# Kernel tuning notes

Hardware: AMD Instinct MI355X
Metric: run time of the kernel (lower is better)

## Reference

```python
import jax, jax.numpy as jnp
import numpy as np

D_MODEL = 1024
NUM_HEADS = 16
D_K = D_MODEL // NUM_HEADS


def setup_inputs() -> dict:
    key = jax.random.key(0)
    ks = jax.random.split(key, 12)
    B, S, D = 2, 2048, D_MODEL
    s = 1.0 / np.sqrt(D)
    inp = {
        "Q": jax.random.normal(ks[0], (B, S, D), jnp.float32),
        "K": jax.random.normal(ks[1], (B, S, D), jnp.float32),
        "V": jax.random.normal(ks[2], (B, S, D), jnp.float32),
        "Wq": jax.random.normal(ks[3], (D, D), jnp.float32) * s,
        "bq": jax.random.normal(ks[4], (D,), jnp.float32) * s,
        "Wk": jax.random.normal(ks[5], (D, D), jnp.float32) * s,
        "bk": jax.random.normal(ks[6], (D,), jnp.float32) * s,
        "Wv": jax.random.normal(ks[7], (D, D), jnp.float32) * s,
        "bv": jax.random.normal(ks[8], (D,), jnp.float32) * s,
        "Wo": jax.random.normal(ks[9], (D, D), jnp.float32) * s,
        "bo": jax.random.normal(ks[10], (D,), jnp.float32) * s,
    }
    return inp


def _split_heads(x, B, S):
    # [B, S, D] -> [B, H, S, d_k]
    return x.reshape(B, S, NUM_HEADS, D_K).transpose(0, 2, 1, 3)


def reference(Q, K, V, Wq, bq, Wk, bk, Wv, bv, Wo, bo):
    B, S, D = Q.shape
    # torch nn.Linear: y = x @ W.T + b
    q = _split_heads(Q @ Wq.T + bq, B, S)
    k = _split_heads(K @ Wk.T + bk, B, S)
    v = _split_heads(V @ Wv.T + bv, B, S)
    scale = 1.0 / np.sqrt(D_K).astype(np.float32)
    # [B, H, S, S] attention scores (materialized, as in the original)
    scores = jnp.einsum('bhqd,bhkd->bhqk', q, k) * scale
    probs = jax.nn.softmax(scores, axis=-1)
    out = jnp.einsum('bhqk,bhkd->bhqd', probs, v)
    out = out.transpose(0, 2, 1, 3).reshape(B, S, D)
    return out @ Wo.T + bo
```

## Files before the change

### kernel.cpp

```cpp
#include <hip/hip_runtime.h>
#include <hip/hip_bf16.h>

#define S_LEN   2048
#define NHEADS  16
#define DKH     64
#define DMODEL  1024
#define NBATCH  2

typedef __bf16 bf16x8 __attribute__((ext_vector_type(8)));
typedef __bf16 bf16x4 __attribute__((ext_vector_type(4)));
typedef float  f32x4  __attribute__((ext_vector_type(4)));

typedef __attribute__((address_space(3))) void       lds_void;
typedef const __attribute__((address_space(1))) void glob_void;

__device__ __forceinline__ void glds16(const void* g, void* l) {
    __builtin_amdgcn_global_load_lds((glob_void*)g, (lds_void*)l, 16, 0, 0);
}

struct CvtArgs {
    const float* src[7];
    __bf16*      dst[7];
    int          n[7];
};

__global__ __launch_bounds__(256)
void cvt_all_k(CvtArgs a)
{
    const int t = blockIdx.y;
    const size_t i = ((size_t)blockIdx.x * 256 + threadIdx.x) * 8;
    if ((int)i >= a.n[t]) return;
    const float* s = a.src[t];
    f32x4 lo = *(const f32x4*)(s + i);
    f32x4 hi = *(const f32x4*)(s + i + 4);
    bf16x8 r;
#pragma unroll
    for (int k = 0; k < 4; ++k) { r[k] = (__bf16)lo[k]; r[4 + k] = (__bf16)hi[k]; }
    *(bf16x8*)(a.dst[t] + i) = r;
}

__device__ __forceinline__ void gemm_core(
    const __bf16* __restrict__ A, const __bf16* __restrict__ W,
    int m0, int n0, int K,
    __bf16 (*As)[32], __bf16 (*Ws)[32], f32x4 acc[4][4])
{
    const int tid  = threadIdx.x;
    const int lane = tid & 63;
    const int wv   = tid >> 6;
    const int l15  = lane & 15;
    const int quad = lane >> 4;
    const int wm   = wv >> 1;
    const int wn   = wv & 1;
    const int grow = lane >> 2;
    const int gcol = (lane & 3) * 8;

    const __bf16* ag0 = A + (size_t)(m0 + wv * 32 + grow) * K + gcol;
    const __bf16* ag1 = A + (size_t)(m0 + wv * 32 + 16 + grow) * K + gcol;
    const __bf16* wg0 = W + (size_t)(n0 + wv * 32 + grow) * K + gcol;
    const __bf16* wg1 = W + (size_t)(n0 + wv * 32 + 16 + grow) * K + gcol;
    void* al0 = &As[wv * 32][0];
    void* al1 = &As[wv * 32 + 16][0];
    void* wl0 = &Ws[wv * 32][0];
    void* wl1 = &Ws[wv * 32 + 16][0];

    for (int k0 = 0;;) {
        __syncthreads();
        glds16(ag0 + k0, al0);
        glds16(ag1 + k0, al1);
        glds16(wg0 + k0, wl0);
        glds16(wg1 + k0, wl1);
        __syncthreads();

        bf16x8 af[4], wf[4];
#pragma unroll
        for (int i = 0; i < 4; ++i)
            af[i] = *(const bf16x8*)&As[wm * 64 + i * 16 + l15][quad * 8];
#pragma unroll
        for (int j = 0; j < 4; ++j)
            wf[j] = *(const bf16x8*)&Ws[wn * 64 + j * 16 + l15][quad * 8];
#pragma unroll
        for (int i = 0; i < 4; ++i)
#pragma unroll
            for (int j = 0; j < 4; ++j)
                acc[i][j] = __builtin_amdgcn_mfma_f32_16x16x32_bf16(af[i], wf[j], acc[i][j], 0, 0, 0);

        k0 += 32;
        if (k0 >= K) break;
    }
}

struct GArgs {
    const __bf16* A[3];
    const __bf16* W[3];
    const float*  bias[3];
    __bf16*       out[3];
};

__global__ __launch_bounds__(256)
void gemm_qkv(GArgs g, int z_off)
{
    __shared__ __align__(16) __bf16 As[128][32];
    __shared__ __align__(16) __bf16 Ws[128][32];

    const int fid = blockIdx.x;
    const int z   = (fid >> 8) + z_off;
    const int l   = fid & 255;
    const int x   = l & 7;
    const int t   = l >> 3;
    int m0, n0;
    if (z == 2) { m0 = (t & 7) * 128;          n0 = (x * 4 + (t >> 3)) * 128; }
    else        { m0 = (x * 4 + (t & 3)) * 128; n0 = (t >> 2) * 128; }

    f32x4 acc[4][4];
#pragma unroll
    for (int i = 0; i < 4; ++i)
#pragma unroll
        for (int j = 0; j < 4; ++j) acc[i][j] = (f32x4){0.f, 0.f, 0.f, 0.f};

    gemm_core(g.A[z], g.W[z], m0, n0, DMODEL, As, Ws, acc);

    const int lane = threadIdx.x & 63;
    const int wv   = threadIdx.x >> 6;
    const int l15  = lane & 15;
    const int quad = lane >> 4;
    const int wm   = wv >> 1;
    const int wn   = wv & 1;
    const float* bias = g.bias[z];
    __bf16* out = g.out[z];
    const float oscale = (z == 0) ? 0.125f : 1.0f;

#pragma unroll
    for (int j = 0; j < 4; ++j) {
        const int col = n0 + wn * 64 + j * 16 + l15;
        const float bcol = (z == 2) ? 0.f : bias[col];
#pragma unroll
        for (int i = 0; i < 4; ++i) {
#pragma unroll
            for (int r = 0; r < 4; ++r) {
                const int row = m0 + wm * 64 + i * 16 + quad * 4 + r;
                size_t idx;
                float v = acc[i][j][r];
                if (z == 2) {
                    const int h = row >> 6, d = row & (DKH - 1);
                    const int b = col >> 11, s = col & (S_LEN - 1);
                    v += bias[row];
                    idx = ((size_t)(b * NHEADS + h) * DKH + d) * S_LEN + s;
                } else {
                    const int b = row >> 11, s = row & (S_LEN - 1);
                    const int h = col >> 6, d = col & (DKH - 1);
                    v = (v + bcol) * oscale;
                    idx = ((size_t)(b * NHEADS + h) * S_LEN + s) * DKH + d;
                }
                out[idx] = (__bf16)v;
            }
        }
    }
}

__global__ __launch_bounds__(256)
void gemm_out(const __bf16* __restrict__ A, const __bf16* __restrict__ W,
              const float* __restrict__ bias, float* __restrict__ out)
{
    __shared__ __align__(16) __bf16 As[128][32];
    __shared__ __align__(16) __bf16 Ws[128][32];

    const int fid = blockIdx.x;
    const int x = fid & 7;
    const int t = fid >> 3;
    const int m0 = (x * 4 + (t & 3)) * 128;
    const int n0 = (t >> 2) * 128;

    f32x4 acc[4][4];
#pragma unroll
    for (int i = 0; i < 4; ++i)
#pragma unroll
        for (int j = 0; j < 4; ++j) acc[i][j] = (f32x4){0.f, 0.f, 0.f, 0.f};

    gemm_core(A, W, m0, n0, DMODEL, As, Ws, acc);

    const int lane = threadIdx.x & 63;
    const int wv   = threadIdx.x >> 6;
    const int l15  = lane & 15;
    const int quad = lane >> 4;
    const int wm   = wv >> 1;
    const int wn   = wv & 1;

#pragma unroll
    for (int j = 0; j < 4; ++j) {
        const int col = n0 + wn * 64 + j * 16 + l15;
        const float bv = bias[col];
#pragma unroll
        for (int i = 0; i < 4; ++i)
#pragma unroll
            for (int r = 0; r < 4; ++r) {
                const int row = m0 + wm * 64 + i * 16 + quad * 4 + r;
                out[(size_t)row * DMODEL + col] = acc[i][j][r] + bv;
            }
    }
}

__global__ __launch_bounds__(256, 2)
void attn_k(const __bf16* __restrict__ Qh, const __bf16* __restrict__ Kh,
            const __bf16* __restrict__ VhT, __bf16* __restrict__ out)
{
    __shared__ __align__(16) __bf16 Ks[128][72];
    __shared__ __align__(16) __bf16 Vs[64][136];

    const int tid  = threadIdx.x;
    const int lane = tid & 63;
    const int wv   = tid >> 6;
    const int l15  = lane & 15;
    const int quad = lane >> 4;

    const int fid = blockIdx.x;
    const int x  = fid & 7;
    const int j  = fid >> 3;
    const int bh = x * 4 + (j & 3);
    const int q0 = (j >> 2) * 128;
    const int b  = bh >> 4;
    const int h  = bh & (NHEADS - 1);

    const __bf16* Q  = Qh  + (size_t)bh * S_LEN * DKH;
    const __bf16* Kp = Kh  + (size_t)bh * S_LEN * DKH;
    const __bf16* Vt = VhT + (size_t)bh * DKH * S_LEN;

    bf16x8 qa[2][2];
#pragma unroll
    for (int u = 0; u < 2; ++u) {
        const int qrow = q0 + wv * 32 + u * 16 + l15;
        qa[u][0] = *(const bf16x8*)(Q + (size_t)qrow * DKH + quad * 8);
        qa[u][1] = *(const bf16x8*)(Q + (size_t)qrow * DKH + quad * 8 + 32);
    }

    const int krow = tid >> 1, kcb = (tid & 1) * 32;
    const int vrow = tid >> 2, vcb = (tid & 3) * 32;
    const __bf16* kst = Kp + (size_t)krow * DKH   + kcb;
    const __bf16* vst = Vt + (size_t)vrow * S_LEN + vcb;

    f32x4 oT[2][4];
#pragma unroll
    for (int u = 0; u < 2; ++u)
#pragma unroll
        for (int jt = 0; jt < 4; ++jt) oT[u][jt] = (f32x4){0.f, 0.f, 0.f, 0.f};
    float lacc[2] = {0.f, 0.f};

    bf16x8 kreg[4], vperm[4];
    {
        bf16x8 vr[4];
#pragma unroll
        for (int p = 0; p < 4; ++p) {
            kreg[p] = *(const bf16x8*)(kst + p * 8);
            vr[p]   = *(const bf16x8*)(vst + p * 8);
        }
#pragma unroll
        for (int p = 0; p < 4; ++p) {
            const int G = (p >> 1), e = (p & 1) * 4;
#pragma unroll
            for (int s = 0; s < 4; ++s) {
                vperm[p][s]     = vr[G][e + s];
                vperm[p][4 + s] = vr[G + 2][e + s];
            }
        }
    }

    for (int kt = 0; kt < S_LEN; kt += 128) {
        __syncthreads();
#pragma unroll
        for (int p = 0; p < 4; ++p) {
            *(bf16x8*)&Ks[krow][kcb + p * 8] = kreg[p];
            *(bf16x8*)&Vs[vrow][vcb + p * 8] = vperm[p];
        }
        __syncthreads();
        if (kt + 128 < S_LEN) {
            bf16x8 vr[4];
#pragma unroll
            for (int p = 0; p < 4; ++p) {
                kreg[p] = *(const bf16x8*)(kst + (size_t)(kt + 128) * DKH + p * 8);
                vr[p]   = *(const bf16x8*)(vst + kt + 128 + p * 8);
            }
#pragma unroll
            for (int p = 0; p < 4; ++p) {
                const int G = (p >> 1), e = (p & 1) * 4;
#pragma unroll
                for (int s = 0; s < 4; ++s) {
                    vperm[p][s]     = vr[G][e + s];
                    vperm[p][4 + s] = vr[G + 2][e + s];
                }
            }
        }

#pragma unroll
        for (int ht = 0; ht < 2; ++ht) {
            float p[2][4][4];
#pragma unroll
            for (int n = 0; n < 4; ++n) {
                bf16x8 kA = *(const bf16x8*)&Ks[ht * 64 + n * 16 + l15][quad * 8];
                bf16x8 kB = *(const bf16x8*)&Ks[ht * 64 + n * 16 + l15][quad * 8 + 32];
#pragma unroll
                for (int u = 0; u < 2; ++u) {
                    f32x4 st = {0.f, 0.f, 0.f, 0.f};
                    st = __builtin_amdgcn_mfma_f32_16x16x32_bf16(kA, qa[u][0], st, 0, 0, 0);
                    st = __builtin_amdgcn_mfma_f32_16x16x32_bf16(kB, qa[u][1], st, 0, 0, 0);
#pragma unroll
                    for (int r = 0; r < 4; ++r) {
                        p[u][n][r] = __expf(st[r]);
                        lacc[u] += p[u][n][r];
                    }
                }
            }

#pragma unroll
            for (int t = 0; t < 2; ++t) {
                bf16x8 pf[2];
#pragma unroll
                for (int u = 0; u < 2; ++u)
#pragma unroll
                    for (int s = 0; s < 4; ++s) {
                        pf[u][s]     = (__bf16)p[u][2 * t][s];
                        pf[u][4 + s] = (__bf16)p[u][2 * t + 1][s];
                    }
#pragma unroll
                for (int jt = 0; jt < 4; ++jt) {
                    bf16x8 vf = *(const bf16x8*)&Vs[jt * 16 + l15][ht * 64 + t * 32 + quad * 8];
#pragma unroll
                    for (int u = 0; u < 2; ++u)
                        oT[u][jt] = __builtin_amdgcn_mfma_f32_16x16x32_bf16(vf, pf[u], oT[u][jt], 0, 0, 0);
                }
            }
        }
    }

#pragma unroll
    for (int u = 0; u < 2; ++u) {
        float l = lacc[u];
        l += __shfl_xor(l, 16);
        l += __shfl_xor(l, 32);
        const float inv = 1.0f / l;
        __bf16* op = out + ((size_t)b * S_LEN + q0 + wv * 32 + u * 16 + l15) * DMODEL + h * DKH;
#pragma unroll
        for (int jt = 0; jt < 4; ++jt) {
            bf16x4 t;
#pragma unroll
            for (int r = 0; r < 4; ++r) t[r] = (__bf16)(oT[u][jt][r] * inv);
            *(bf16x4*)(op + jt * 16 + quad * 4) = t;
        }
    }
}

extern "C" void kernel_launch(void* const* d_in, const int* in_sizes, int n_in,
                              void* d_out, int out_size, void* d_ws, size_t ws_size,
                              hipStream_t stream) {
    const float* Qi = (const float*)d_in[0];
    const float* Ki = (const float*)d_in[1];
    const float* Vi = (const float*)d_in[2];
    const float* Wq = (const float*)d_in[3];
    const float* bq = (const float*)d_in[4];
    const float* Wk = (const float*)d_in[5];
    const float* bk = (const float*)d_in[6];
    const float* Wv = (const float*)d_in[7];
    const float* bv = (const float*)d_in[8];
    const float* Wo = (const float*)d_in[9];
    const float* bo = (const float*)d_in[10];
    float* out = (float*)d_out;

    const int M = NBATCH * S_LEN;
    const size_t NW = (size_t)DMODEL * DMODEL;
    const size_t NE = (size_t)M * DMODEL;
    const bool big = ws_size >= ((size_t)56 << 20);

    __bf16* w_bf   = (__bf16*)d_ws;
    __bf16* Qin_bf = w_bf + 4 * NW;
    __bf16* Kin_bf = Qin_bf + NE;
    __bf16* Vin_bf = Kin_bf + NE;
    __bf16* q_ws   = Vin_bf + NE;
    __bf16* k_ws   = q_ws + NE;
    __bf16* vT_ws   = big ? (k_ws + NE) : Kin_bf;
    __bf16* attn_ws = Qin_bf;
    __bf16* wq_bf = w_bf, *wk_bf = w_bf + NW, *wv_bf = w_bf + 2 * NW, *wo_bf = w_bf + 3 * NW;

    CvtArgs ca;
    ca.src[0] = Wq; ca.src[1] = Wk; ca.src[2] = Wv; ca.src[3] = Wo;
    ca.src[4] = Qi; ca.src[5] = Ki; ca.src[6] = Vi;
    ca.dst[0] = wq_bf; ca.dst[1] = wk_bf; ca.dst[2] = wv_bf; ca.dst[3] = wo_bf;
    ca.dst[4] = Qin_bf; ca.dst[5] = Kin_bf; ca.dst[6] = Vin_bf;
    for (int t = 0; t < 4; ++t) ca.n[t] = (int)NW;
    for (int t = 4; t < 7; ++t) ca.n[t] = (int)NE;
    cvt_all_k<<<dim3(2048, 7), 256, 0, stream>>>(ca);

    GArgs g;
    g.A[0] = Qin_bf; g.W[0] = wq_bf;  g.bias[0] = bq; g.out[0] = q_ws;
    g.A[1] = Kin_bf; g.W[1] = wk_bf;  g.bias[1] = bk; g.out[1] = k_ws;
    g.A[2] = wv_bf;  g.W[2] = Vin_bf; g.bias[2] = bv; g.out[2] = vT_ws;
    if (big) {
        gemm_qkv<<<dim3(768), 256, 0, stream>>>(g, 0);
    } else {
        gemm_qkv<<<dim3(512), 256, 0, stream>>>(g, 0);
        gemm_qkv<<<dim3(256), 256, 0, stream>>>(g, 2);
    }

    attn_k<<<dim3(512), 256, 0, stream>>>(q_ws, k_ws, vT_ws, attn_ws);

    gemm_out<<<dim3(256), 256, 0, stream>>>(attn_ws, wo_bf, bo, out);
}
```

Baseline: 246.3 us.

## Fuse fp32-to-bf16 activation conversion into QKV GEMM tile loads

The fp32 activations Q, K and V are no longer converted to bf16 in a separate pass. The QKV GEMM now loads fp32 tiles into registers, prefetching the next k-slice, then converts them and writes bf16 to LDS. The separate conversion kernel shrinks to the weights only, and the workspace layout and the single 768-block launch are simplified. This removes a full read-write pass over about 50 MB of activations. In exchange the GEMM reads fp32 (twice the bytes per tile) and loses the async global-to-LDS path for those operands, and fp32 tiles are re-read by every block along N.

```diff
diff --git a/kernel.cpp b/kernel.cpp
--- a/kernel.cpp
+++ b/kernel.cpp
@@ -18,29 +18,26 @@
     __builtin_amdgcn_global_load_lds((glob_void*)g, (lds_void*)l, 16, 0, 0);
 }
 
-struct CvtArgs {
-    const float* src[7];
-    __bf16*      dst[7];
-    int          n[7];
-};
-
 __global__ __launch_bounds__(256)
-void cvt_all_k(CvtArgs a)
+void cvt_w_k(const float* __restrict__ wq, const float* __restrict__ wk,
+             const float* __restrict__ wv, const float* __restrict__ wo,
+             __bf16* __restrict__ dst)
 {
-    const int t = blockIdx.y;
+    const float* srcs[4] = {wq, wk, wv, wo};
+    const float* s = srcs[blockIdx.y];
+    __bf16* d = dst + (size_t)blockIdx.y * (DMODEL * DMODEL);
     const size_t i = ((size_t)blockIdx.x * 256 + threadIdx.x) * 8;
-    if ((int)i >= a.n[t]) return;
-    const float* s = a.src[t];
     f32x4 lo = *(const f32x4*)(s + i);
     f32x4 hi = *(const f32x4*)(s + i + 4);
     bf16x8 r;
 #pragma unroll
     for (int k = 0; k < 4; ++k) { r[k] = (__bf16)lo[k]; r[4 + k] = (__bf16)hi[k]; }
-    *(bf16x8*)(a.dst[t] + i) = r;
-}
-
+    *(bf16x8*)(d + i) = r;
+}
+
+template<bool AF32, bool WF32>
 __device__ __forceinline__ void gemm_core(
-    const __bf16* __restrict__ A, const __bf16* __restrict__ W,
+    const void* __restrict__ Ap, const void* __restrict__ Wp,
     int m0, int n0, int K,
     __bf16 (*As)[32], __bf16 (*Ws)[32], f32x4 acc[4][4])
 {
@@ -54,22 +51,70 @@
     const int grow = lane >> 2;
     const int gcol = (lane & 3) * 8;
 
-    const __bf16* ag0 = A + (size_t)(m0 + wv * 32 + grow) * K + gcol;
-    const __bf16* ag1 = A + (size_t)(m0 + wv * 32 + 16 + grow) * K + gcol;
-    const __bf16* wg0 = W + (size_t)(n0 + wv * 32 + grow) * K + gcol;
-    const __bf16* wg1 = W + (size_t)(n0 + wv * 32 + 16 + grow) * K + gcol;
+    const __bf16* ag0 = (const __bf16*)Ap + (size_t)(m0 + wv * 32 + grow) * K + gcol;
+    const __bf16* ag1 = (const __bf16*)Ap + (size_t)(m0 + wv * 32 + 16 + grow) * K + gcol;
+    const __bf16* wg0 = (const __bf16*)Wp + (size_t)(n0 + wv * 32 + grow) * K + gcol;
+    const __bf16* wg1 = (const __bf16*)Wp + (size_t)(n0 + wv * 32 + 16 + grow) * K + gcol;
     void* al0 = &As[wv * 32][0];
     void* al1 = &As[wv * 32 + 16][0];
     void* wl0 = &Ws[wv * 32][0];
     void* wl1 = &Ws[wv * 32 + 16][0];
 
+    const int fr = tid >> 1;
+    const int fc = (tid & 1) * 16;
+    const float* afp = (const float*)Ap + (size_t)(m0 + fr) * K + fc;
+    const float* wfp = (const float*)Wp + (size_t)(n0 + fr) * K + fc;
+
+    f32x4 apf[4], wpf[4];
+    if (AF32) {
+#pragma unroll
+        for (int t = 0; t < 4; ++t) apf[t] = *(const f32x4*)(afp + t * 4);
+    }
+    if (WF32) {
+#pragma unroll
+        for (int t = 0; t < 4; ++t) wpf[t] = *(const f32x4*)(wfp + t * 4);
+    }
+
     for (int k0 = 0;;) {
         __syncthreads();
-        glds16(ag0 + k0, al0);
-        glds16(ag1 + k0, al1);
-        glds16(wg0 + k0, wl0);
-        glds16(wg1 + k0, wl1);
+        if (AF32) {
+            bf16x8 v0, v1;
+#pragma unroll
+            for (int t = 0; t < 4; ++t) {
+                v0[t] = (__bf16)apf[0][t]; v0[4 + t] = (__bf16)apf[1][t];
+                v1[t] = (__bf16)apf[2][t]; v1[4 + t] = (__bf16)apf[3][t];
+            }
+            *(bf16x8*)&As[fr][fc]     = v0;
+            *(bf16x8*)&As[fr][fc + 8] = v1;
+        } else {
+            glds16(ag0 + k0, al0);
+            glds16(ag1 + k0, al1);
+        }
+        if (WF32) {
+            bf16x8 v0, v1;
+#pragma unroll
+            for (int t = 0; t < 4; ++t) {
+                v0[t] = (__bf16)wpf[0][t]; v0[4 + t] = (__bf16)wpf[1][t];
+                v1[t] = (__bf16)wpf[2][t]; v1[4 + t] = (__bf16)wpf[3][t];
+            }
+            *(bf16x8*)&Ws[fr][fc]     = v0;
+            *(bf16x8*)&Ws[fr][fc + 8] = v1;
+        } else {
+            glds16(wg0 + k0, wl0);
+            glds16(wg1 + k0, wl1);
+        }
         __syncthreads();
+        k0 += 32;
+        if (k0 < K) {
+            if (AF32) {
+#pragma unroll
+                for (int t = 0; t < 4; ++t) apf[t] = *(const f32x4*)(afp + k0 + t * 4);
+            }
+            if (WF32) {
+#pragma unroll
+                for (int t = 0; t < 4; ++t) wpf[t] = *(const f32x4*)(wfp + k0 + t * 4);
+            }
+        }
 
         bf16x8 af[4], wf[4];
 #pragma unroll
@@ -84,31 +129,30 @@
             for (int j = 0; j < 4; ++j)
                 acc[i][j] = __builtin_amdgcn_mfma_f32_16x16x32_bf16(af[i], wf[j], acc[i][j], 0, 0, 0);
 
-        k0 += 32;
         if (k0 >= K) break;
     }
 }
 
 struct GArgs {
-    const __bf16* A[3];
-    const __bf16* W[3];
-    const float*  bias[3];
-    __bf16*       out[3];
+    const void* A[3];
+    const void* W[3];
+    const float* bias[3];
+    __bf16*     out[3];
 };
 
 __global__ __launch_bounds__(256)
-void gemm_qkv(GArgs g, int z_off)
+void gemm_qkv(GArgs g)
 {
     __shared__ __align__(16) __bf16 As[128][32];
     __shared__ __align__(16) __bf16 Ws[128][32];
 
     const int fid = blockIdx.x;
-    const int z   = (fid >> 8) + z_off;
+    const int z   = fid >> 8;
     const int l   = fid & 255;
     const int x   = l & 7;
     const int t   = l >> 3;
     int m0, n0;
-    if (z == 2) { m0 = (t & 7) * 128;          n0 = (x * 4 + (t >> 3)) * 128; }
+    if (z == 2) { m0 = (t & 7) * 128;           n0 = (x * 4 + (t >> 3)) * 128; }
     else        { m0 = (x * 4 + (t & 3)) * 128; n0 = (t >> 2) * 128; }
 
     f32x4 acc[4][4];
@@ -117,7 +161,8 @@
 #pragma unroll
         for (int j = 0; j < 4; ++j) acc[i][j] = (f32x4){0.f, 0.f, 0.f, 0.f};
 
-    gemm_core(g.A[z], g.W[z], m0, n0, DMODEL, As, Ws, acc);
+    if (z == 2) gemm_core<false, true>(g.A[2], g.W[2], m0, n0, DMODEL, As, Ws, acc);
+    else        gemm_core<true, false>(g.A[z], g.W[z], m0, n0, DMODEL, As, Ws, acc);
 
     const int lane = threadIdx.x & 63;
     const int wv   = threadIdx.x >> 6;
@@ -176,7 +221,7 @@
 #pragma unroll
         for (int j = 0; j < 4; ++j) acc[i][j] = (f32x4){0.f, 0.f, 0.f, 0.f};
 
-    gemm_core(A, W, m0, n0, DMODEL, As, Ws, acc);
+    gemm_core<false, false>(A, W, m0, n0, DMODEL, As, Ws, acc);
 
     const int lane = threadIdx.x & 63;
     const int wv   = threadIdx.x >> 6;
@@ -363,40 +408,22 @@
     const float* bo = (const float*)d_in[10];
     float* out = (float*)d_out;
 
-    const int M = NBATCH * S_LEN;
     const size_t NW = (size_t)DMODEL * DMODEL;
-    const size_t NE = (size_t)M * DMODEL;
-    const bool big = ws_size >= ((size_t)56 << 20);
-
-    __bf16* w_bf   = (__bf16*)d_ws;
-    __bf16* Qin_bf = w_bf + 4 * NW;
-    __bf16* Kin_bf = Qin_bf + NE;
-    __bf16* Vin_bf = Kin_bf + NE;
-    __bf16* q_ws   = Vin_bf + NE;
-    __bf16* k_ws   = q_ws + NE;
-    __bf16* vT_ws   = big ? (k_ws + NE) : Kin_bf;
-    __bf16* attn_ws = Qin_bf;
+    const size_t NE = (size_t)NBATCH * S_LEN * DMODEL;
+    __bf16* w_bf    = (__bf16*)d_ws;
+    __bf16* q_ws    = w_bf + 4 * NW;
+    __bf16* k_ws    = q_ws + NE;
+    __bf16* vT_ws   = k_ws + NE;
+    __bf16* attn_ws = vT_ws + NE;
     __bf16* wq_bf = w_bf, *wk_bf = w_bf + NW, *wv_bf = w_bf + 2 * NW, *wo_bf = w_bf + 3 * NW;
 
-    CvtArgs ca;
-    ca.src[0] = Wq; ca.src[1] = Wk; ca.src[2] = Wv; ca.src[3] = Wo;
-    ca.src[4] = Qi; ca.src[5] = Ki; ca.src[6] = Vi;
-    ca.dst[0] = wq_bf; ca.dst[1] = wk_bf; ca.dst[2] = wv_bf; ca.dst[3] = wo_bf;
-    ca.dst[4] = Qin_bf; ca.dst[5] = Kin_bf; ca.dst[6] = Vin_bf;
-    for (int t = 0; t < 4; ++t) ca.n[t] = (int)NW;
-    for (int t = 4; t < 7; ++t) ca.n[t] = (int)NE;
-    cvt_all_k<<<dim3(2048, 7), 256, 0, stream>>>(ca);
+    cvt_w_k<<<dim3(512, 4), 256, 0, stream>>>(Wq, Wk, Wv, Wo, w_bf);
 
     GArgs g;
-    g.A[0] = Qin_bf; g.W[0] = wq_bf;  g.bias[0] = bq; g.out[0] = q_ws;
-    g.A[1] = Kin_bf; g.W[1] = wk_bf;  g.bias[1] = bk; g.out[1] = k_ws;
-    g.A[2] = wv_bf;  g.W[2] = Vin_bf; g.bias[2] = bv; g.out[2] = vT_ws;
-    if (big) {
-        gemm_qkv<<<dim3(768), 256, 0, stream>>>(g, 0);
-    } else {
-        gemm_qkv<<<dim3(512), 256, 0, stream>>>(g, 0);
-        gemm_qkv<<<dim3(256), 256, 0, stream>>>(g, 2);
-    }
+    g.A[0] = Qi;    g.W[0] = wq_bf; g.bias[0] = bq; g.out[0] = q_ws;
+    g.A[1] = Ki;    g.W[1] = wk_bf; g.bias[1] = bk; g.out[1] = k_ws;
+    g.A[2] = wv_bf; g.W[2] = Vi;    g.bias[2] = bv; g.out[2] = vT_ws;
+    gemm_qkv<<<dim3(768), 256, 0, stream>>>(g);
 
     attn_k<<<dim3(512), 256, 0, stream>>>(q_ws, k_ws, vT_ws, attn_ws);
 
```

Measured after the change: 266.8 us. 8.3% more time.
